# Kernel tuning notes

Hardware: AMD Instinct MI355X
Metric: run time of the kernel (lower is better)

## Reference

```python
import jax, jax.numpy as jnp
import numpy as np

D_MODEL = 2048
N_HEADS = 16
D_K = D_MODEL // N_HEADS
BATCH = 4
SEQ = 2048


def setup_inputs() -> dict:
    key = jax.random.key(0)
    ks = jax.random.split(key, 9)
    s = 1.0 / np.sqrt(D_MODEL)
    return {
        "x": jax.random.normal(ks[0], (BATCH, SEQ, D_MODEL), dtype=jnp.float32),
        "wq_w": jax.random.normal(ks[1], (D_MODEL, D_MODEL), dtype=jnp.float32) * s,
        "wq_b": jax.random.normal(ks[2], (D_MODEL,), dtype=jnp.float32) * 0.02,
        "wk_w": jax.random.normal(ks[3], (D_MODEL, D_MODEL), dtype=jnp.float32) * s,
        "wk_b": jax.random.normal(ks[4], (D_MODEL,), dtype=jnp.float32) * 0.02,
        "wv_w": jax.random.normal(ks[5], (D_MODEL, D_MODEL), dtype=jnp.float32) * s,
        "wv_b": jax.random.normal(ks[6], (D_MODEL,), dtype=jnp.float32) * 0.02,
        "wo_w": jax.random.normal(ks[7], (D_MODEL, D_MODEL), dtype=jnp.float32) * s,
        "wo_b": jax.random.normal(ks[8], (D_MODEL,), dtype=jnp.float32) * 0.02,
    }


def reference(x, wq_w, wq_b, wk_w, wk_b, wv_w, wv_b, wo_w, wo_b):
    b, s, _ = x.shape
    # Linear projections (torch Linear: x @ W^T + b)
    def split_heads(t):  # (b, s, d_model) -> (b, h, s, d_k)
        return t.reshape(b, s, N_HEADS, D_K).transpose(0, 2, 1, 3)
    q = split_heads(x @ wq_w.T + wq_b)
    k = split_heads(x @ wk_w.T + wk_b)
    v = split_heads(x @ wv_w.T + wv_b)
    scale = 1.0 / jnp.sqrt(jnp.asarray(D_K, dtype=x.dtype))
    scores = jnp.einsum("bhqd,bhkd->bhqk", q, k) * scale  # (b, h, s, s)
    attn = jax.nn.softmax(scores, axis=-1)
    ctx = jnp.einsum("bhqk,bhkd->bhqd", attn, v)
    ctx = ctx.transpose(0, 2, 1, 3).reshape(b, s, D_MODEL)
    out = ctx @ wo_w.T + wo_b
    return out
```

## Files before the change

kernel.cpp:

```cpp
#include <hip/hip_runtime.h>
#include <hip/hip_bf16.h>
#include <math.h>

typedef __attribute__((ext_vector_type(8))) short short8;
typedef __attribute__((ext_vector_type(4))) float f32x4;
typedef __attribute__((ext_vector_type(16))) float f32x16;
typedef __attribute__((ext_vector_type(4))) unsigned short u16x4;
typedef __attribute__((ext_vector_type(8))) unsigned short u16x8;
typedef __attribute__((ext_vector_type(4))) unsigned int u32x4;
typedef __attribute__((ext_vector_type(2))) int i32x2;
typedef unsigned short u16;
typedef unsigned int u32;

#define DM 2048
#define SQ 2048
#define NB 4
#define NH 16
#define DKH 128
#define KT 64
#define NT (SQ / KT)

__device__ __forceinline__ u16 f2bf(float f) {
  unsigned u = __float_as_uint(f);
  u += 0x7fffu + ((u >> 16) & 1u);
  return (u16)(u >> 16);
}

__device__ __forceinline__ u32 cvtpk(float lo, float hi) {
  u32 r;
  asm("v_cvt_pk_bf16_f32 %0, %1, %2" : "=v"(r) : "v"(lo), "v"(hi));
  return r;
}

__device__ __forceinline__ void gload16(const u16* g, u16* lds) {
  __builtin_amdgcn_global_load_lds(
      (const __attribute__((address_space(1))) unsigned int*)g,
      (__attribute__((address_space(3))) unsigned int*)lds, 16, 0, 0);
}

__global__ void cvt_bf16(const float* __restrict__ in, u16* __restrict__ out, int n) {
  int i = (blockIdx.x * blockDim.x + threadIdx.x) * 4;
  if (i >= n) return;
  float4 v = *(const float4*)(in + i);
  u16x4 o;
  o.x = f2bf(v.x); o.y = f2bf(v.y); o.z = f2bf(v.z); o.w = f2bf(v.w);
  *(u16x4*)(out + i) = o;
}

__global__ void cvt_w4(const float* __restrict__ w0, const float* __restrict__ w1,
                       const float* __restrict__ w2, const float* __restrict__ w3,
                       u16* __restrict__ dst) {
  const int sel = blockIdx.y;
  const float* src;
  switch (sel) {
    case 0: src = w0; break;
    case 1: src = w1; break;
    case 2: src = w2; break;
    default: src = w3; break;
  }
  const int i = (blockIdx.x * blockDim.x + threadIdx.x) * 4;
  float4 v = *(const float4*)(src + i);
  u16x4 o;
  o.x = f2bf(v.x); o.y = f2bf(v.y); o.z = f2bf(v.z); o.w = f2bf(v.w);
  *(u16x4*)(dst + (size_t)sel * DM * DM + i) = o;
}


#define VM8 asm volatile("s_waitcnt vmcnt(8)" ::: "memory")
#define VM4 asm volatile("s_waitcnt vmcnt(4)" ::: "memory")
#define VM0 asm volatile("s_waitcnt vmcnt(0)" ::: "memory")

#define STAGE(T)                                                        \
  do {                                                                  \
    const size_t ko_ = (size_t)(T) * 32;                                \
    const int bb_ = ((T) & 3) * 8192;                                   \
    gload16(Abase + ko_, &smA[bb_ + w * 1024]);                         \
    gload16(Abase + (size_t)16 * K + ko_, &smA[bb_ + w * 1024 + 512]);  \
    gload16(Bbase + ko_, &smB[bb_ + w * 1024]);                         \
    gload16(Bbase + (size_t)16 * K + ko_, &smB[bb_ + w * 1024 + 512]);  \
  } while (0)

#define GITER(T, VMOP, DOSTG)                                                          \
  do {                                                                                 \
    const int bi_ = (T) & 3;                                                           \
    const u16* pA_ = &smA[bi_ * 8192];                                                 \
    const u16* pB_ = &smB[bi_ * 8192];                                                 \
    short8 af_[2][4], bf_[2][2];                                                       \
    _Pragma("unroll") for (int kk = 0; kk < 2; ++kk) {                                 \
      const int sl_ = (((kk << 1) | hi) ^ (c5 & 3)) << 3;                              \
      _Pragma("unroll") for (int mf = 0; mf < 4; ++mf)                                 \
        af_[kk][mf] = *(const short8*)&pA_[(wr * 128 + mf * 32 + c5) * 32 + sl_];      \
      _Pragma("unroll") for (int nf = 0; nf < 2; ++nf)                                 \
        bf_[kk][nf] = *(const short8*)&pB_[(wc * 64 + nf * 32 + c5) * 32 + sl_];       \
    }                                                                                  \
    if (DOSTG) STAGE((T) + 3);                                                         \
    __builtin_amdgcn_s_barrier();                                                      \
    asm volatile("s_waitcnt lgkmcnt(0)" ::: "memory");                                 \
    __builtin_amdgcn_sched_barrier(0);                                                 \
    __builtin_amdgcn_s_setprio(1);                                                     \
    _Pragma("unroll") for (int kk = 0; kk < 2; ++kk)                                   \
      _Pragma("unroll") for (int mf = 0; mf < 4; ++mf)                                 \
        _Pragma("unroll") for (int nf = 0; nf < 2; ++nf)                               \
          acc[mf][nf] =                                                                \
              __builtin_amdgcn_mfma_f32_32x32x16_bf16(af_[kk][mf], bf_[kk][nf],        \
                                                      acc[mf][nf], 0, 0, 0);           \
    __builtin_amdgcn_s_setprio(0);                                                     \
    VMOP;                                                                              \
    __builtin_amdgcn_s_barrier();                                                      \
  } while (0)

template <bool OUTF32>
__global__ __launch_bounds__(512, 2) void gemm_bt2(
    const u16* __restrict__ A, const u16* __restrict__ B,
    const float* __restrict__ bias, void* __restrict__ Cout,
    int M, int N, int K, float oscale) {
  __shared__ u16 smA[4 * 8192];
  __shared__ u16 smB[4 * 8192];
  const int tid = threadIdx.x;
  const int w = tid >> 6, l = tid & 63;
  const int c5 = l & 31, hi = l >> 5;
  const int wr = w >> 2, wc = w & 3;
  const int m0 = blockIdx.y * 256, n0 = blockIdx.x * 256;
  const int NSTEP = K / 32;

  f32x16 acc[4][2] = {};

  const int srow = w * 32 + (l >> 2);
  const int scol = ((l & 3) ^ ((l >> 2) & 3)) * 8;
  const u16* Abase = A + (size_t)(m0 + srow) * K + scol;
  const u16* Bbase = B + (size_t)(n0 + srow) * K + scol;

  STAGE(0); STAGE(1); STAGE(2);
  VM8;
  __builtin_amdgcn_s_barrier();

  for (int t = 0; t < NSTEP - 3; ++t) GITER(t, VM8, true);
  GITER(NSTEP - 3, VM4, false);
  GITER(NSTEP - 2, VM0, false);
  GITER(NSTEP - 1, ((void)0), false);

#pragma unroll
  for (int nf = 0; nf < 2; ++nf) {
    const int col = n0 + wc * 64 + nf * 32 + c5;
    const float bv = bias[col];
#pragma unroll
    for (int mf = 0; mf < 4; ++mf) {
#pragma unroll
      for (int r = 0; r < 16; ++r) {
        const int row = m0 + wr * 128 + mf * 32 + (r & 3) + 8 * (r >> 2) + 4 * hi;
        const float v = (acc[mf][nf][r] + bv) * oscale;
        if (OUTF32)
          ((float*)Cout)[(size_t)row * N + col] = v;
        else
          ((u16*)Cout)[(size_t)row * N + col] = f2bf(v);
      }
    }
  }
}

__global__ __launch_bounds__(512, 2) void attn(
    const u16* __restrict__ Q, const u16* __restrict__ K,
    const u16* __restrict__ V, u16* __restrict__ O) {
  __shared__ u16 smK[2 * 8192];
  __shared__ u16 smV[2 * 9216];
  __shared__ float alScr[8 * 32];

  const int tid = threadIdx.x;
  const int w = tid >> 6, l = tid & 63;
  const int c5 = l & 31, hi = l >> 5;

  int flat = blockIdx.x + ((int)blockIdx.y << 3) + ((int)blockIdx.z << 7);
  flat = (flat & 7) * 64 + (flat >> 3);
  const int qt = flat & 7, h = (flat >> 3) & 15, b = flat >> 7;

  const int q0 = qt * 256 + w * 32;
  const size_t rowb = (size_t)b * SQ;
  const int hoff = h * DKH;

  short8 qf[8];
#pragma unroll
  for (int ds = 0; ds < 8; ++ds)
    qf[ds] = *(const short8*)&Q[(rowb + q0 + c5) * DM + hoff + ds * 16 + hi * 8];

  f32x16 o[4] = {};
  float mrow = -1e30f, lsum = 0.f;

  const int vdg = tid >> 5;
  const int kvp = (tid & 31) * 2;
  u16x8 va, vb;

  {
    const u16* vp = &V[(rowb + kvp) * DM + hoff + vdg * 8];
    va = *(const u16x8*)vp;
    vb = *(const u16x8*)(vp + DM);
#pragma unroll
    for (int uu = 0; uu < 2; ++uu) {
      const int u = w * 2 + uu;
      const int row = u * 4 + (l >> 4);
      const int col16 = (l & 15) ^ (row & 15);
      gload16(&K[(rowb + row) * DM + hoff + col16 * 8], &smK[u * 512]);
    }
#pragma unroll
    for (int i = 0; i < 8; ++i) {
      const int d = vdg * 8 + i;
      *(u32*)&smV[d * 72 + kvp] = (u32)va[i] | ((u32)vb[i] << 16);
    }
  }
  __syncthreads();

  int buf = 0;
  for (int t = 0; t < NT; ++t) {
    const int nb = buf ^ 1;
    if (t + 1 < NT) {
      const size_t kvr = rowb + (size_t)(t + 1) * KT;
      const u16* vp = &V[(kvr + kvp) * DM + hoff + vdg * 8];
      va = *(const u16x8*)vp;
      vb = *(const u16x8*)(vp + DM);
#pragma unroll
      for (int uu = 0; uu < 2; ++uu) {
        const int u = w * 2 + uu;
        const int row = u * 4 + (l >> 4);
        const int col16 = (l & 15) ^ (row & 15);
        gload16(&K[(kvr + row) * DM + hoff + col16 * 8], &smK[nb * 8192 + u * 512]);
      }
    }

    f32x16 s[2] = {};
    __builtin_amdgcn_s_setprio(1);
#pragma unroll
    for (int ni = 0; ni < 2; ++ni) {
      const int row = ni * 32 + c5;
#pragma unroll
      for (int ds = 0; ds < 8; ++ds) {
        const short8 kf = *(const short8*)&smK[buf * 8192 + row * 128 + (((ds << 1) | hi) ^ (row & 15)) * 8];
        s[ni] = __builtin_amdgcn_mfma_f32_32x32x16_bf16(kf, qf[ds], s[ni], 0, 0, 0);
      }
    }
    __builtin_amdgcn_s_setprio(0);

    float mx = s[0][0];
#pragma unroll
    for (int ni = 0; ni < 2; ++ni)
#pragma unroll
      for (int i = 0; i < 16; ++i)
        mx = fmaxf(mx, s[ni][i]);
    i32x2 sw = __builtin_amdgcn_permlane32_swap(__float_as_int(mx), __float_as_int(mx), false, false);
    const float gmax = fmaxf(__int_as_float(sw.x), __int_as_float(sw.y));

    if (__any(gmax > mrow + 10.0f)) {
      const float mn = fmaxf(mrow, gmax);
      const float al = exp2f(mrow - mn);
      mrow = mn;
      lsum *= al;
      alScr[w * 32 + c5] = al;
#pragma unroll
      for (int r = 0; r < 16; ++r) {
        const float av = alScr[w * 32 + (r & 3) + 8 * (r >> 2) + 4 * hi];
#pragma unroll
        for (int dg = 0; dg < 4; ++dg) o[dg][r] *= av;
      }
    }

    float ps0 = 0.f, ps1 = 0.f;
#pragma unroll
    for (int i = 0; i < 16; ++i) {
      const float p0 = exp2f(s[0][i] - mrow);
      const float p1 = exp2f(s[1][i] - mrow);
      s[0][i] = p0; s[1][i] = p1;
      ps0 += p0; ps1 += p1;
    }
    lsum += ps0 + ps1;

    __builtin_amdgcn_s_setprio(1);
#pragma unroll
    for (int ks = 0; ks < 4; ++ks) {
      const int b0 = (ks & 1) * 8;
      const int ni = ks >> 1;
      const u32 A0 = cvtpk(s[ni][b0 + 0], s[ni][b0 + 1]);
      const u32 A1 = cvtpk(s[ni][b0 + 4], s[ni][b0 + 5]);
      const u32 B0 = cvtpk(s[ni][b0 + 2], s[ni][b0 + 3]);
      const u32 B1 = cvtpk(s[ni][b0 + 6], s[ni][b0 + 7]);
      const i32x2 r0 = __builtin_amdgcn_permlane32_swap((int)A0, (int)A1, false, false);
      const i32x2 r1 = __builtin_amdgcn_permlane32_swap((int)B0, (int)B1, false, false);
      u32x4 paw;
      paw.x = (u32)r0.x; paw.y = (u32)r1.x; paw.z = (u32)r0.y; paw.w = (u32)r1.y;
      const short8 pa = *(const short8*)&paw;
#pragma unroll
      for (int dg = 0; dg < 4; ++dg) {
        const int rowd = dg * 32 + c5;
        const short8 vf = *(const short8*)&smV[buf * 9216 + rowd * 72 + ks * 16 + hi * 8];
        o[dg] = __builtin_amdgcn_mfma_f32_32x32x16_bf16(pa, vf, o[dg], 0, 0, 0);
      }
    }
    __builtin_amdgcn_s_setprio(0);

    if (t + 1 < NT) {
#pragma unroll
      for (int i = 0; i < 8; ++i) {
        const int d = vdg * 8 + i;
        *(u32*)&smV[nb * 9216 + d * 72 + kvp] = (u32)va[i] | ((u32)vb[i] << 16);
      }
    }
    __syncthreads();
    buf = nb;
  }

  {
    const i32x2 sl = __builtin_amdgcn_permlane32_swap(__float_as_int(lsum), __float_as_int(lsum), false, false);
    const float tot = __int_as_float(sl.x) + __int_as_float(sl.y);
    alScr[w * 32 + c5] = 1.0f / tot;
  }
#pragma unroll
  for (int r = 0; r < 16; ++r) {
    const int qloc = (r & 3) + 8 * (r >> 2) + 4 * hi;
    const float inv = alScr[w * 32 + qloc];
    const size_t orow = (rowb + q0 + qloc) * DM + hoff;
#pragma unroll
    for (int dg = 0; dg < 4; ++dg)
      O[orow + dg * 32 + c5] = f2bf(o[dg][r] * inv);
  }
}

extern "C" void kernel_launch(void* const* d_in, const int* in_sizes, int n_in,
                              void* d_out, int out_size, void* d_ws, size_t ws_size,
                              hipStream_t stream) {
  const float* x    = (const float*)d_in[0];
  const float* wq_w = (const float*)d_in[1];
  const float* wq_b = (const float*)d_in[2];
  const float* wk_w = (const float*)d_in[3];
  const float* wk_b = (const float*)d_in[4];
  const float* wv_w = (const float*)d_in[5];
  const float* wv_b = (const float*)d_in[6];
  const float* wo_w = (const float*)d_in[7];
  const float* wo_b = (const float*)d_in[8];
  float* out = (float*)d_out;

  u16* p = (u16*)d_ws;
  u16* xb  = p; p += (size_t)NB * SQ * DM;
  u16* wqb = p; p += (size_t)DM * DM;
  u16* wkb = p; p += (size_t)DM * DM;
  u16* wvb = p; p += (size_t)DM * DM;
  u16* wob = p; p += (size_t)DM * DM;
  u16* Qb  = p; p += (size_t)NB * SQ * DM;
  u16* Kb  = p; p += (size_t)NB * SQ * DM;
  u16* Vb  = p; p += (size_t)NB * SQ * DM;
  u16* ctx = xb;

  const int nx = NB * SQ * DM;
  cvt_bf16<<<dim3(nx / 1024), dim3(256), 0, stream>>>(x, xb, nx);
  cvt_w4<<<dim3(DM * DM / 1024, 4), dim3(256), 0, stream>>>(wq_w, wk_w, wv_w, wo_w, wqb);

  const float sc2 = 0.08838834764831845f * 1.4426950408889634f;
  dim3 gg(DM / 256, (NB * SQ) / 256);
  gemm_bt2<false><<<gg, dim3(512), 0, stream>>>(xb, wqb, wq_b, Qb, NB * SQ, DM, DM, sc2);
  gemm_bt2<false><<<gg, dim3(512), 0, stream>>>(xb, wkb, wk_b, Kb, NB * SQ, DM, DM, 1.0f);
  gemm_bt2<false><<<gg, dim3(512), 0, stream>>>(xb, wvb, wv_b, Vb, NB * SQ, DM, DM, 1.0f);

  attn<<<dim3(SQ / 256, NH, NB), dim3(512), 0, stream>>>(Qb, Kb, Vb, ctx);

  gemm_bt2<true><<<gg, dim3(512), 0, stream>>>(ctx, wob, wo_b, out, NB * SQ, DM, DM, 1.0f);
}
```

Before: 617.5 us.

## Rewrite projection GEMM as 8-phase ping-pong pipeline with XCD-aware block remap

Replaces the 4-stage K=32 GEMM main loop with a double-buffered K=64 loop split into four quadrant phases. Each phase interleaves LDS fragment reads, half-tile global prefetches and a block of MFMAs between barriers, and the LDS swizzle widens to 8 groups. It also remaps the flat workgroup index so consecutive tiles land on the same XCD, aiming for better L2 reuse. The goal is to overlap memory with MFMA more finely, at the cost of more barriers per K step and more complex vmcnt accounting.

```diff
diff --git a/kernel.cpp b/kernel.cpp
--- a/kernel.cpp
+++ b/kernel.cpp
@@ -66,78 +66,113 @@
 }
 
 
-#define VM8 asm volatile("s_waitcnt vmcnt(8)" ::: "memory")
-#define VM4 asm volatile("s_waitcnt vmcnt(4)" ::: "memory")
-#define VM0 asm volatile("s_waitcnt vmcnt(0)" ::: "memory")
-
-#define STAGE(T)                                                        \
-  do {                                                                  \
-    const size_t ko_ = (size_t)(T) * 32;                                \
-    const int bb_ = ((T) & 3) * 8192;                                   \
-    gload16(Abase + ko_, &smA[bb_ + w * 1024]);                         \
-    gload16(Abase + (size_t)16 * K + ko_, &smA[bb_ + w * 1024 + 512]);  \
-    gload16(Bbase + ko_, &smB[bb_ + w * 1024]);                         \
-    gload16(Bbase + (size_t)16 * K + ko_, &smB[bb_ + w * 1024 + 512]);  \
+#define STG_A(T, HALF)                                                \
+  do {                                                                \
+    u16* d_ = &smA[((T) & 1) * 16384 + (((HALF) * 128 + w * 16) << 6)]; \
+    const u16* s_ = As + (size_t)((HALF) * 128) * K + (size_t)(T) * 64; \
+    gload16(s_, d_);                                                  \
+    gload16(s_ + (size_t)8 * K, d_ + 8 * 64);                         \
   } while (0)
 
-#define GITER(T, VMOP, DOSTG)                                                          \
-  do {                                                                                 \
-    const int bi_ = (T) & 3;                                                           \
-    const u16* pA_ = &smA[bi_ * 8192];                                                 \
-    const u16* pB_ = &smB[bi_ * 8192];                                                 \
-    short8 af_[2][4], bf_[2][2];                                                       \
-    _Pragma("unroll") for (int kk = 0; kk < 2; ++kk) {                                 \
-      const int sl_ = (((kk << 1) | hi) ^ (c5 & 3)) << 3;                              \
-      _Pragma("unroll") for (int mf = 0; mf < 4; ++mf)                                 \
-        af_[kk][mf] = *(const short8*)&pA_[(wr * 128 + mf * 32 + c5) * 32 + sl_];      \
-      _Pragma("unroll") for (int nf = 0; nf < 2; ++nf)                                 \
-        bf_[kk][nf] = *(const short8*)&pB_[(wc * 64 + nf * 32 + c5) * 32 + sl_];       \
-    }                                                                                  \
-    if (DOSTG) STAGE((T) + 3);                                                         \
-    __builtin_amdgcn_s_barrier();                                                      \
-    asm volatile("s_waitcnt lgkmcnt(0)" ::: "memory");                                 \
-    __builtin_amdgcn_sched_barrier(0);                                                 \
-    __builtin_amdgcn_s_setprio(1);                                                     \
-    _Pragma("unroll") for (int kk = 0; kk < 2; ++kk)                                   \
-      _Pragma("unroll") for (int mf = 0; mf < 4; ++mf)                                 \
-        _Pragma("unroll") for (int nf = 0; nf < 2; ++nf)                               \
-          acc[mf][nf] =                                                                \
-              __builtin_amdgcn_mfma_f32_32x32x16_bf16(af_[kk][mf], bf_[kk][nf],        \
-                                                      acc[mf][nf], 0, 0, 0);           \
-    __builtin_amdgcn_s_setprio(0);                                                     \
-    VMOP;                                                                              \
-    __builtin_amdgcn_s_barrier();                                                      \
+#define STG_B(T, HALF)                                                \
+  do {                                                                \
+    u16* d_ = &smB[((T) & 1) * 16384 + (((HALF) * 128 + w * 16) << 6)]; \
+    const u16* s_ = Bs + (size_t)((HALF) * 128) * K + (size_t)(T) * 64; \
+    gload16(s_, d_);                                                  \
+    gload16(s_ + (size_t)8 * K, d_ + 8 * 64);                         \
   } while (0)
 
+#define LDA(QM)                                                          \
+  do {                                                                   \
+    const u16* p_ = &smA[bi * 16384 + ((wr * 128 + (QM) * 64 + c5) << 6)]; \
+    _Pragma("unroll") for (int s = 0; s < 4; ++s) {                      \
+      const int sl_ = (((s << 1) | hi) ^ (c5 & 7)) << 3;                 \
+      af[0][s] = *(const short8*)&p_[sl_];                               \
+      af[1][s] = *(const short8*)&p_[32 * 64 + sl_];                     \
+    }                                                                    \
+  } while (0)
+
+#define LDB(QN)                                                          \
+  do {                                                                   \
+    const u16* p_ = &smB[bi * 16384 + ((wc * 64 + (QN) * 32 + c5) << 6)]; \
+    _Pragma("unroll") for (int s = 0; s < 4; ++s)                        \
+      bf[QN][s] = *(const short8*)&p_[(((s << 1) | hi) ^ (c5 & 7)) << 3]; \
+  } while (0)
+
+#define MFMA_Q(QM, QN)                                                             \
+  __builtin_amdgcn_s_setprio(1);                                                   \
+  _Pragma("unroll") for (int s = 0; s < 4; ++s) {                                  \
+    acc[(QM) * 2][(QN)] = __builtin_amdgcn_mfma_f32_32x32x16_bf16(                 \
+        af[0][s], bf[QN][s], acc[(QM) * 2][(QN)], 0, 0, 0);                        \
+    acc[(QM) * 2 + 1][(QN)] = __builtin_amdgcn_mfma_f32_32x32x16_bf16(             \
+        af[1][s], bf[QN][s], acc[(QM) * 2 + 1][(QN)], 0, 0, 0);                    \
+  }                                                                                \
+  __builtin_amdgcn_s_setprio(0);
+
+#define WAIT_LGKM                                         \
+  asm volatile("s_waitcnt lgkmcnt(0)" ::: "memory");      \
+  __builtin_amdgcn_sched_barrier(0);
+
 template <bool OUTF32>
-__global__ __launch_bounds__(512, 2) void gemm_bt2(
+__global__ __launch_bounds__(512, 2) void gemm8p(
     const u16* __restrict__ A, const u16* __restrict__ B,
     const float* __restrict__ bias, void* __restrict__ Cout,
     int M, int N, int K, float oscale) {
-  __shared__ u16 smA[4 * 8192];
-  __shared__ u16 smB[4 * 8192];
+  __shared__ u16 smA[2 * 16384];
+  __shared__ u16 smB[2 * 16384];
   const int tid = threadIdx.x;
   const int w = tid >> 6, l = tid & 63;
   const int c5 = l & 31, hi = l >> 5;
   const int wr = w >> 2, wc = w & 3;
-  const int m0 = blockIdx.y * 256, n0 = blockIdx.x * 256;
-  const int NSTEP = K / 32;
-
+
+  int flat = blockIdx.x + (int)gridDim.x * (int)blockIdx.y;
+  const int nwg = (int)(gridDim.x * gridDim.y);
+  flat = (flat & 7) * (nwg >> 3) + (flat >> 3);
+  const int m0 = (flat / (int)gridDim.x) * 256, n0 = (flat % (int)gridDim.x) * 256;
+
+  const int NSTEP = K / 64;
   f32x16 acc[4][2] = {};
 
-  const int srow = w * 32 + (l >> 2);
-  const int scol = ((l & 3) ^ ((l >> 2) & 3)) * 8;
-  const u16* Abase = A + (size_t)(m0 + srow) * K + scol;
-  const u16* Bbase = B + (size_t)(n0 + srow) * K + scol;
-
-  STAGE(0); STAGE(1); STAGE(2);
-  VM8;
+  const int sgrp = l >> 3;
+  const int scol = ((l & 7) ^ sgrp) * 8;
+  const u16* As = A + (size_t)(m0 + w * 16 + sgrp) * K + scol;
+  const u16* Bs = B + (size_t)(n0 + w * 16 + sgrp) * K + scol;
+
+  STG_A(0, 0); STG_A(0, 1); STG_B(0, 0); STG_B(0, 1);
+  STG_B(1, 0); STG_A(1, 0);
+  asm volatile("s_waitcnt vmcnt(4)" ::: "memory");
   __builtin_amdgcn_s_barrier();
 
-  for (int t = 0; t < NSTEP - 3; ++t) GITER(t, VM8, true);
-  GITER(NSTEP - 3, VM4, false);
-  GITER(NSTEP - 2, VM0, false);
-  GITER(NSTEP - 1, ((void)0), false);
+  short8 af[2][4], bf[2][4];
+  for (int t = 0; t < NSTEP; ++t) {
+    const int bi = t & 1;
+    LDA(0); LDB(0);
+    if (t + 1 < NSTEP) STG_B(t + 1, 1);
+    __builtin_amdgcn_s_barrier();
+    WAIT_LGKM;
+    MFMA_Q(0, 0);
+    __builtin_amdgcn_s_barrier();
+    LDB(1);
+    if (t + 1 < NSTEP) STG_A(t + 1, 1);
+    __builtin_amdgcn_s_barrier();
+    WAIT_LGKM;
+    MFMA_Q(0, 1);
+    __builtin_amdgcn_s_barrier();
+    LDA(1);
+    if (t + 2 < NSTEP) STG_B(t + 2, 0);
+    __builtin_amdgcn_s_barrier();
+    WAIT_LGKM;
+    MFMA_Q(1, 1);
+    __builtin_amdgcn_s_barrier();
+    if (t + 2 < NSTEP) STG_A(t + 2, 0);
+    __builtin_amdgcn_s_barrier();
+    MFMA_Q(1, 0);
+    if (t + 2 < NSTEP)
+      asm volatile("s_waitcnt vmcnt(4)" ::: "memory");
+    else if (t + 1 < NSTEP)
+      asm volatile("s_waitcnt vmcnt(0)" ::: "memory");
+    __builtin_amdgcn_s_barrier();
+  }
 
 #pragma unroll
   for (int nf = 0; nf < 2; ++nf) {
@@ -352,11 +387,11 @@
 
   const float sc2 = 0.08838834764831845f * 1.4426950408889634f;
   dim3 gg(DM / 256, (NB * SQ) / 256);
-  gemm_bt2<false><<<gg, dim3(512), 0, stream>>>(xb, wqb, wq_b, Qb, NB * SQ, DM, DM, sc2);
-  gemm_bt2<false><<<gg, dim3(512), 0, stream>>>(xb, wkb, wk_b, Kb, NB * SQ, DM, DM, 1.0f);
-  gemm_bt2<false><<<gg, dim3(512), 0, stream>>>(xb, wvb, wv_b, Vb, NB * SQ, DM, DM, 1.0f);
+  gemm8p<false><<<gg, dim3(512), 0, stream>>>(xb, wqb, wq_b, Qb, NB * SQ, DM, DM, sc2);
+  gemm8p<false><<<gg, dim3(512), 0, stream>>>(xb, wkb, wk_b, Kb, NB * SQ, DM, DM, 1.0f);
+  gemm8p<false><<<gg, dim3(512), 0, stream>>>(xb, wvb, wv_b, Vb, NB * SQ, DM, DM, 1.0f);
 
   attn<<<dim3(SQ / 256, NH, NB), dim3(512), 0, stream>>>(Qb, Kb, Vb, ctx);
 
-  gemm_bt2<true><<<gg, dim3(512), 0, stream>>>(ctx, wob, wo_b, out, NB * SQ, DM, DM, 1.0f);
-}
+  gemm8p<true><<<gg, dim3(512), 0, stream>>>(ctx, wob, wo_b, out, NB * SQ, DM, DM, 1.0f);
+}
```

Measured after the change: 563.6 us. 8.7% less time.
